# Optimization experiments

Hardware: AMD Instinct MI355X
Metric: run time of the kernel (lower is better)

## Reference

```python
import jax, jax.numpy as jnp
import numpy as np

B, T, P, D = 8, 2048, 4, 768

def setup_inputs() -> dict:
    key = jax.random.key(0)
    k1, k2, k3 = jax.random.split(key, 3)
    text_inputs = jax.random.normal(k1, (B, T, D), dtype=jnp.float32)
    sit_mask = jax.random.randint(k2, (B, T), 0, 2).astype(jnp.float32)
    proposition_matrix = jax.random.normal(k3, (B, T, P, D), dtype=jnp.float32)
    return {"text_inputs": text_inputs, "sit_mask": sit_mask, "proposition_matrix": proposition_matrix}

def reference(text_inputs, sit_mask, proposition_matrix):
    # D from proposition_matrix (matches text hidden dim), used for softmax scaling
    d = proposition_matrix.shape[-1]
    t = text_inputs.shape[1]
    # raw scores [B,T,T], scaled by 1/sqrt(D)
    scores = jnp.einsum('bid,bjd->bij', text_inputs, text_inputs) * (1.0 / jnp.sqrt(jnp.asarray(d, text_inputs.dtype)))
    # causal mask: strictly upper triangular -> -inf (tokens attend to self + past)
    causal = jnp.tril(jnp.ones((t, t), dtype=bool))  # [T,T]
    scores = jnp.where(causal[None, :, :], scores, -jnp.inf)
    weights = jax.nn.softmax(scores, axis=2)
    # padding mask via outer product of sit_mask; zero AFTER softmax (no renorm), as in original
    pad = (sit_mask[:, :, None] * sit_mask[:, None, :]) != 0  # [B,T,T]
    weights = jnp.where(pad, weights, jnp.zeros((), weights.dtype))
    out = jnp.einsum('bij,bjd->bid', weights, text_inputs)  # [B,T,D]
    # concat_self_hidden=True
    out = jnp.concatenate([out, text_inputs], axis=-1)  # [B,T,2D]
    return out
```

## Files before the change

kernel.cpp:

```cpp
#include <hip/hip_runtime.h>
#include <math.h>

constexpr int kT = 2048;
constexpr int kD = 768;
constexpr int kTileShorts = 16 * kD;
constexpr int kTilesPerBatch = kT / 16;

typedef __attribute__((ext_vector_type(8))) short short8;
typedef __attribute__((ext_vector_type(4))) float f32x4;
typedef __attribute__((ext_vector_type(16))) float f32x16;

#define FB(f) __builtin_bit_cast(unsigned, (f))
__device__ __forceinline__ unsigned pk_hi16(unsigned hi, unsigned lo) {
  return __builtin_amdgcn_perm(hi, lo, 0x07060302);
}
__device__ __forceinline__ unsigned pk_lo16(unsigned hi, unsigned lo) {
  return __builtin_amdgcn_perm(hi, lo, 0x05040100);
}

__device__ __forceinline__ void lds_barrier() {
  asm volatile("" ::: "memory");
  __builtin_amdgcn_s_waitcnt(0xC07F);
  __builtin_amdgcn_s_barrier();
  asm volatile("" ::: "memory");
}

__device__ __forceinline__ void gload_lds16(const void* g, void* l) {
  __builtin_amdgcn_global_load_lds(
      (const __attribute__((address_space(1))) unsigned int*)g,
      (__attribute__((address_space(3))) unsigned int*)l, 16, 0, 0);
}

__global__ __launch_bounds__(256) void prep_bf16(
    const float* __restrict__ x,
    unsigned short* __restrict__ xbf, unsigned short* __restrict__ xvt)
{
  const int tid = threadIdx.x;
  const int w = tid >> 6, l = tid & 63;
  const int l15 = l & 15, q4 = l >> 4;
  const int bt = (int)blockIdx.x;
  const float* xb = x + (size_t)bt * 16 * kD;
  unsigned short* ob = xbf + (size_t)bt * kTileShorts;
  unsigned short* ov = xvt + (size_t)bt * kTileShorts;

#pragma unroll
  for (int it = 0; it < 3; ++it) {
    const int dq = l15 + 16 * it + 48 * w;
    unsigned lo[4], hi[4];
#pragma unroll
    for (int jj = 0; jj < 4; ++jj) {
      const float4 f = *(const float4*)(xb + (size_t)(q4 + 4 * jj) * kD + 4 * dq);
      lo[jj] = pk_hi16(FB(f.y), FB(f.x));
      hi[jj] = pk_hi16(FB(f.w), FB(f.z));
    }
    const int dp = 4 * (l15 + 16 * it);
    const int g = dp >> 3, e0 = dp & 7;
#pragma unroll
    for (int jj = 0; jj < 4; ++jj) {
      const int j = q4 + 4 * jj;
      uint2 v; v.x = lo[jj]; v.y = hi[jj];
      *(uint2*)&ob[w * 3072 + j * 192 + ((g ^ (j & 7)) << 3) + e0] = v;
    }
    const int jb = (4 * q4) ^ (8 * ((dq >> 2) & 1));
    const int base = dq * 64 + jb;
    uint2 v;
    v.x = pk_lo16(lo[1], lo[0]); v.y = pk_lo16(lo[3], lo[2]);
    *(uint2*)&ov[base + ((0 ^ (dq & 3)) << 4)] = v;
    v.x = pk_hi16(lo[1], lo[0]); v.y = pk_hi16(lo[3], lo[2]);
    *(uint2*)&ov[base + ((1 ^ (dq & 3)) << 4)] = v;
    v.x = pk_lo16(hi[1], hi[0]); v.y = pk_lo16(hi[3], hi[2]);
    *(uint2*)&ov[base + ((2 ^ (dq & 3)) << 4)] = v;
    v.x = pk_hi16(hi[1], hi[0]); v.y = pk_hi16(hi[3], hi[2]);
    *(uint2*)&ov[base + ((3 ^ (dq & 3)) << 4)] = v;
  }
}

__global__ __launch_bounds__(256, 2) void attn_mfma5(
    const float* __restrict__ x, const float* __restrict__ mask,
    const unsigned short* __restrict__ xbf,
    const unsigned short* __restrict__ xvt,
    float* __restrict__ out, float* __restrict__ ml)
{
  const int tid = threadIdx.x;
  const int w = tid >> 6, l = tid & 63;
  const int l15 = l & 15, q4 = l >> 4;
  const int l31 = l & 31, h2 = l >> 5;

  const int bid = (int)blockIdx.x;
  const int b = bid & 7;
  const int s = bid >> 3;
  int qq, t0, t1, mode;
  if (s < 80) {
    int g = (s * 2) / 5;
    if (g > 31) g = 31;
    while (g < 31 && (2 * (g + 1) + ((g + 2) >> 1)) <= s) ++g;
    while (g > 0 && (2 * g + ((g + 1) >> 1)) > s) --g;
    const int r = s - (2 * g + ((g + 1) >> 1));
    if (r < 2) {
      qq = 63 - g;
      const int H = qq + 1;
      mode = 1 + r;
      t0 = (r == 0) ? 0 : H;
      t1 = (r == 0) ? H : 2 * H;
    } else {
      qq = 31 - (g >> 1);
      mode = 0; t0 = 0; t1 = 2 * qq + 2;
    }
  } else {
    qq = 15 - (s - 80);
    mode = 0; t0 = 0; t1 = 2 * qq + 2;
  }
  const int i0 = qq << 5;

  const float* xb = x + (size_t)b * kT * kD;
  const float* mrow = mask + (size_t)b * kT;
  const unsigned short* xbfB = xbf + (size_t)b * kTilesPerBatch * kTileShorts;
  const unsigned short* xvtB = xvt + (size_t)b * kTilesPerBatch * kTileShorts;

  __shared__ unsigned short xKc[12288];
  __shared__ unsigned short VTb[12288];
  __shared__ float sPart[2][4][16][36];
  __shared__ unsigned short Pm[2][32][16];
  __shared__ float corrS[2][32];
  __shared__ float invlS[32];
  __shared__ float msk[kT];

  {
    const char* msrc = (const char*)mrow + 2048 * w;
    char* mdst = (char*)&msk[512 * w];
    gload_lds16(msrc + 16 * l, mdst);
    gload_lds16(msrc + 1024 + 16 * l, mdst + 1024);
  }

  short8 qf[2][6];
#pragma unroll
  for (int mt = 0; mt < 2; ++mt) {
    const int tq = (i0 >> 4) + mt;
    const unsigned short* tp = xbfB + (size_t)tq * kTileShorts + w * 3072 + l15 * 192;
#pragma unroll
    for (int s6 = 0; s6 < 6; ++s6)
      qf[mt][s6] = *(const short8*)&tp[((4 * s6 + q4) ^ (l15 & 7)) << 3];
  }

  f32x16 o[6];
#pragma unroll
  for (int nt = 0; nt < 6; ++nt)
#pragma unroll
    for (int e = 0; e < 16; ++e) o[nt][e] = 0.0f;

  float mrun = -INFINITY, lrun = 0.0f;
  const float scale = 0.036084391824351615f;

  const int q = tid & 7, sr = tid >> 3;
  const int jA = (q >> 1) + 8 * (q & 1);
  const int irow = i0 + sr;

  const int D0 = 48 * w + (l31 >> 2);
  const int vtb_off0 = D0 * 64 + (((l31 & 3) ^ (D0 & 3)) << 4)
                     + ((8 * h2) ^ (8 * ((l31 >> 4) & 1)));

  auto stageK = [&](int t) {
    const unsigned short* src = xbfB + (size_t)t * kTileShorts + w * 3072 + 8 * l;
    unsigned short* dst = &xKc[w * 3072];
#pragma unroll
    for (int i = 0; i < 6; ++i) gload_lds16(src + 512 * i, dst + 512 * i);
  };
  auto stageV = [&](int t) {
    const unsigned short* src = xvtB + (size_t)t * kTileShorts + w * 3072 + 8 * l;
    unsigned short* dst = &VTb[w * 3072];
#pragma unroll
    for (int i = 0; i < 6; ++i) gload_lds16(src + 512 * i, dst + 512 * i);
  };

  stageK(t0);
  stageV(t0);
  asm volatile("s_waitcnt vmcnt(12)" ::: "memory");
  lds_barrier();

  for (int t = t0; t < t1; ++t) {
    const int par = t & 1;
    const int j0 = t << 4;

    asm volatile("s_waitcnt vmcnt(6)" ::: "memory");

    {
      f32x4 sf0, sf1;
#pragma unroll
      for (int e = 0; e < 4; ++e) { sf0[e] = 0.f; sf1[e] = 0.f; }
      const unsigned short* kbase = &xKc[w * 3072 + l15 * 192];
#pragma unroll
      for (int s6 = 0; s6 < 6; ++s6) {
        short8 kb = *(const short8*)&kbase[((4 * s6 + q4) ^ (l15 & 7)) << 3];
        sf0 = __builtin_amdgcn_mfma_f32_16x16x32_bf16(qf[0][s6], kb, sf0, 0, 0, 0);
        sf1 = __builtin_amdgcn_mfma_f32_16x16x32_bf16(qf[1][s6], kb, sf1, 0, 0, 0);
      }
      *(f32x4*)&sPart[par][w][l15][4 * q4]      = sf0;
      *(f32x4*)&sPart[par][w][l15][16 + 4 * q4] = sf1;
    }

    if (t + 1 < t1) {
      asm volatile("s_waitcnt lgkmcnt(0)" ::: "memory");
      stageK(t + 1);
    }
    lds_barrier();

    {
      float s0 = 0.f, s1 = 0.f;
#pragma unroll
      for (int ww = 0; ww < 4; ++ww) {
        s0 += sPart[par][ww][jA][sr];
        s1 += sPart[par][ww][jA + 4][sr];
      }
      const float mskA = msk[j0 + jA];
      const float mskB = msk[j0 + jA + 4];
      const int ja = j0 + jA, jb_ = j0 + jA + 4;
      float a0 = (ja  <= irow) ? s0 * scale : -INFINITY;
      float a1 = (jb_ <= irow) ? s1 * scale : -INFINITY;
      float loc = fmaxf(a0, a1);
      loc = fmaxf(loc, __shfl_xor(loc, 1, 64));
      loc = fmaxf(loc, __shfl_xor(loc, 2, 64));
      loc = fmaxf(loc, __shfl_xor(loc, 4, 64));
      const float mn = fmaxf(mrun, loc);
      const float corr = __expf(mrun - mn);
      const float p0 = __expf(a0 - mn);
      const float p1 = __expf(a1 - mn);
      float rs = p0 + p1;
      rs += __shfl_xor(rs, 1, 64);
      rs += __shfl_xor(rs, 2, 64);
      rs += __shfl_xor(rs, 4, 64);
      lrun = lrun * corr + rs;
      mrun = mn;
      const float w0 = (mskA != 0.f) ? p0 : 0.f;
      const float w1 = (mskB != 0.f) ? p1 : 0.f;
      *(unsigned*)&Pm[par][sr][2 * q] = pk_hi16(FB(w1), FB(w0));
      if (q == 0) corrS[par][sr] = corr;
    }
    lds_barrier();

    if (t + 1 < t1) { asm volatile("s_waitcnt vmcnt(6)" ::: "memory"); }
    else            { asm volatile("s_waitcnt vmcnt(0)" ::: "memory"); }

    {
      float cr[16];
#pragma unroll
      for (int e4 = 0; e4 < 4; ++e4) {
        f32x4 qd = *(const f32x4*)&corrS[par][8 * e4 + 4 * h2];
#pragma unroll
        for (int ee = 0; ee < 4; ++ee) cr[4 * e4 + ee] = qd[ee];
      }
#pragma unroll
      for (int nt = 0; nt < 6; ++nt)
#pragma unroll
        for (int e = 0; e < 16; ++e) o[nt][e] *= cr[e];
      short8 pa = *(const short8*)&Pm[par][l31][8 * h2];
#pragma unroll
      for (int nt = 0; nt < 6; ++nt) {
        short8 vb = *(const short8*)&VTb[vtb_off0 + 512 * nt];
        o[nt] = __builtin_amdgcn_mfma_f32_32x32x16_bf16(pa, vb, o[nt], 0, 0, 0);
      }
    }

    if (t + 1 < t1) {
      asm volatile("s_waitcnt lgkmcnt(0)" ::: "memory");
      stageV(t + 1);
    }
  }

  if (mode == 0) {
    if (q == 0) invlS[sr] = (msk[irow] != 0.f) ? 1.0f / lrun : 0.0f;
    lds_barrier();
    float il[16];
#pragma unroll
    for (int e4 = 0; e4 < 4; ++e4) {
      f32x4 qd = *(const f32x4*)&invlS[8 * e4 + 4 * h2];
#pragma unroll
      for (int ee = 0; ee < 4; ++ee) il[4 * e4 + ee] = qd[ee];
    }
    float* ob = out + (size_t)(b * kT + i0) * (2 * kD);
#pragma unroll
    for (int nt = 0; nt < 6; ++nt) {
      const int col = 192 * w + 32 * nt + l31;
#pragma unroll
      for (int e = 0; e < 16; ++e) {
        const int row = (e & 3) + 8 * (e >> 2) + 4 * h2;
        ob[(size_t)row * (2 * kD) + col] = o[nt][e] * il[e];
      }
    }
#pragma unroll
    for (int pass = 0; pass < 2; ++pass) {
      const int rr = (tid >> 4) + 16 * pass;
      const float* srcr = xb + (size_t)(i0 + rr) * kD;
      float* dstr = ob + (size_t)rr * (2 * kD) + kD;
#pragma unroll
      for (int it = 0; it < 12; ++it) {
        const int d4 = (tid & 15) + 16 * it;
        *(float4*)(dstr + 4 * d4) = *(const float4*)(srcr + 4 * d4);
      }
    }
  } else {
    float* ob = out + (size_t)(b * kT + i0) * (2 * kD) + ((mode == 2) ? kD : 0);
#pragma unroll
    for (int nt = 0; nt < 6; ++nt) {
      const int col = 192 * w + 32 * nt + l31;
#pragma unroll
      for (int e = 0; e < 16; ++e) {
        const int row = (e & 3) + 8 * (e >> 2) + 4 * h2;
        ob[(size_t)row * (2 * kD) + col] = o[nt][e];
      }
    }
    if (q == 0) {
      const int base = (((b * 32 + (qq - 32)) * 2 + (mode - 1)) * 64);
      ml[base + sr]      = mrun;
      ml[base + 32 + sr] = lrun;
    }
  }
}

__global__ __launch_bounds__(256) void combine_heavy(
    const float* __restrict__ x, const float* __restrict__ mask,
    const float* __restrict__ ml, float* __restrict__ out)
{
  const int tid = threadIdx.x;
  const int bid = (int)blockIdx.x;
  const int b = bid & 7;
  const int hq = bid >> 3;
  const int i0 = (hq + 32) << 5;
  const float* mrow = mask + (size_t)b * kT;
  const float* mlq = ml + (((size_t)b * 32 + hq) * 2) * 64;

  for (int r = 0; r < 32; ++r) {
    const int i = i0 + r;
    float* orow = out + (size_t)(b * kT + i) * (2 * kD);
    const float* xrow = x + (size_t)(b * kT + i) * kD;
    const float m1 = mlq[r],      l1 = mlq[32 + r];
    const float m2 = mlq[64 + r], l2 = mlq[96 + r];
    const float m = fmaxf(m1, m2);
    const float al = __expf(m1 - m), be = __expf(m2 - m);
    const float lsum = al * l1 + be * l2;
    const float gate = (mrow[i] != 0.f) ? 1.0f / lsum : 0.0f;
    const float ga = gate * al, gb = gate * be;
    if (tid < 192) {
      float4 o1 = *(const float4*)(orow + 4 * tid);
      float4 o2 = *(const float4*)(orow + kD + 4 * tid);
      float4 xv = *(const float4*)(xrow + 4 * tid);
      float4 fo;
      fo.x = ga * o1.x + gb * o2.x;
      fo.y = ga * o1.y + gb * o2.y;
      fo.z = ga * o1.z + gb * o2.z;
      fo.w = ga * o1.w + gb * o2.w;
      *(float4*)(orow + 4 * tid) = fo;
      *(float4*)(orow + kD + 4 * tid) = xv;
    }
  }
}

extern "C" void kernel_launch(void* const* d_in, const int* in_sizes, int n_in,
                              void* d_out, int out_size, void* d_ws, size_t ws_size,
                              hipStream_t stream) {
  const float* x    = (const float*)d_in[0];
  const float* mask = (const float*)d_in[1];
  float* out = (float*)d_out;
  unsigned short* xbf = (unsigned short*)d_ws;
  unsigned short* xvt = xbf + (size_t)8 * kTilesPerBatch * kTileShorts;
  float* ml = (float*)(xvt + (size_t)8 * kTilesPerBatch * kTileShorts);
  prep_bf16<<<dim3(8 * kTilesPerBatch), dim3(256), 0, stream>>>(x, xbf, xvt);
  attn_mfma5<<<dim3(768), dim3(256), 0, stream>>>(x, mask, xbf, xvt, out, ml);
  combine_heavy<<<dim3(256), dim3(256), 0, stream>>>(x, mask, ml, out);
}
```

Baseline: 446.3 us.

## Split attention block across 8 waves and load K/V tiles directly to registers

Doubles the block to 512 threads, with each wave owning half of a D-chunk for QK^T and 96 output columns for PV. The LDS staging of K and V tiles is replaced by direct global-to-register loads, prefetched one tile ahead, and s_setprio is wrapped around the MFMA sections. The goal is more waves per CU to hide latency, lower per-wave register pressure, and less LDS traffic. In exchange, the 8-way score partial reduction adds work, the double-buffered parity is gone, and each lane issues more global loads.

```diff
diff --git a/kernel.cpp b/kernel.cpp
--- a/kernel.cpp
+++ b/kernel.cpp
@@ -75,7 +75,7 @@
   }
 }
 
-__global__ __launch_bounds__(256, 2) void attn_mfma5(
+__global__ __launch_bounds__(512, 4) void attn_mfma6(
     const float* __restrict__ x, const float* __restrict__ mask,
     const unsigned short* __restrict__ xbf,
     const unsigned short* __restrict__ xvt,
@@ -85,6 +85,7 @@
   const int w = tid >> 6, l = tid & 63;
   const int l15 = l & 15, q4 = l >> 4;
   const int l31 = l & 31, h2 = l >> 5;
+  const int cch = w >> 1, hh = w & 1;
 
   const int bid = (int)blockIdx.x;
   const int b = bid & 7;
@@ -117,157 +118,137 @@
   const unsigned short* xbfB = xbf + (size_t)b * kTilesPerBatch * kTileShorts;
   const unsigned short* xvtB = xvt + (size_t)b * kTilesPerBatch * kTileShorts;
 
-  __shared__ unsigned short xKc[12288];
-  __shared__ unsigned short VTb[12288];
-  __shared__ float sPart[2][4][16][36];
-  __shared__ unsigned short Pm[2][32][16];
-  __shared__ float corrS[2][32];
-  __shared__ float invlS[32];
-  __shared__ float msk[kT];
-
+  __shared__ __attribute__((aligned(16))) float sPart[8][16][36];
+  __shared__ __attribute__((aligned(16))) unsigned short Pm[32][16];
+  __shared__ __attribute__((aligned(16))) float corrS[32];
+  __shared__ __attribute__((aligned(16))) float invlS[32];
+  __shared__ __attribute__((aligned(16))) float msk[kT];
+
+  gload_lds16((const char*)mrow + 1024 * w + 16 * l, (char*)&msk[256 * w]);
+
+  int koff[3];
+#pragma unroll
+  for (int s6 = 0; s6 < 3; ++s6) {
+    const int G = (4 * (3 * hh + s6) + q4) ^ (l15 & 7);
+    koff[s6] = cch * 3072 + l15 * 192 + G * 8;
+  }
+
+  short8 qf[2][3];
+#pragma unroll
+  for (int mt = 0; mt < 2; ++mt) {
+    const unsigned short* tp = xbfB + (size_t)((i0 >> 4) + mt) * kTileShorts;
+#pragma unroll
+    for (int s6 = 0; s6 < 3; ++s6)
+      qf[mt][s6] = *(const short8*)&tp[koff[s6]];
+  }
+
+  const int D0 = 24 * w + (l31 >> 2);
+  const int vtb_off0 = D0 * 64 + (((l31 & 3) ^ (D0 & 3)) << 4)
+                     + ((8 * h2) ^ (8 * ((l31 >> 4) & 1)));
+
+  short8 kb[3], vb[3];
   {
-    const char* msrc = (const char*)mrow + 2048 * w;
-    char* mdst = (char*)&msk[512 * w];
-    gload_lds16(msrc + 16 * l, mdst);
-    gload_lds16(msrc + 1024 + 16 * l, mdst + 1024);
-  }
-
-  short8 qf[2][6];
-#pragma unroll
-  for (int mt = 0; mt < 2; ++mt) {
-    const int tq = (i0 >> 4) + mt;
-    const unsigned short* tp = xbfB + (size_t)tq * kTileShorts + w * 3072 + l15 * 192;
-#pragma unroll
-    for (int s6 = 0; s6 < 6; ++s6)
-      qf[mt][s6] = *(const short8*)&tp[((4 * s6 + q4) ^ (l15 & 7)) << 3];
-  }
-
-  f32x16 o[6];
-#pragma unroll
-  for (int nt = 0; nt < 6; ++nt)
+    const unsigned short* kt = xbfB + (size_t)t0 * kTileShorts;
+    const unsigned short* vt = xvtB + (size_t)t0 * kTileShorts;
+#pragma unroll
+    for (int s6 = 0; s6 < 3; ++s6) kb[s6] = *(const short8*)&kt[koff[s6]];
+#pragma unroll
+    for (int nt = 0; nt < 3; ++nt) vb[nt] = *(const short8*)&vt[vtb_off0 + 512 * nt];
+  }
+
+  f32x16 o[3];
+#pragma unroll
+  for (int nt = 0; nt < 3; ++nt)
 #pragma unroll
     for (int e = 0; e < 16; ++e) o[nt][e] = 0.0f;
 
   float mrun = -INFINITY, lrun = 0.0f;
   const float scale = 0.036084391824351615f;
 
-  const int q = tid & 7, sr = tid >> 3;
-  const int jA = (q >> 1) + 8 * (q & 1);
-  const int irow = i0 + sr;
-
-  const int D0 = 48 * w + (l31 >> 2);
-  const int vtb_off0 = D0 * 64 + (((l31 & 3) ^ (D0 & 3)) << 4)
-                     + ((8 * h2) ^ (8 * ((l31 >> 4) & 1)));
-
-  auto stageK = [&](int t) {
-    const unsigned short* src = xbfB + (size_t)t * kTileShorts + w * 3072 + 8 * l;
-    unsigned short* dst = &xKc[w * 3072];
-#pragma unroll
-    for (int i = 0; i < 6; ++i) gload_lds16(src + 512 * i, dst + 512 * i);
-  };
-  auto stageV = [&](int t) {
-    const unsigned short* src = xvtB + (size_t)t * kTileShorts + w * 3072 + 8 * l;
-    unsigned short* dst = &VTb[w * 3072];
-#pragma unroll
-    for (int i = 0; i < 6; ++i) gload_lds16(src + 512 * i, dst + 512 * i);
-  };
-
-  stageK(t0);
-  stageV(t0);
-  asm volatile("s_waitcnt vmcnt(12)" ::: "memory");
-  lds_barrier();
+  const int r = tid >> 4, j = tid & 15;
+  const int irow = i0 + r;
+  const int cst = 4 * (j & 3) + 2 * (j >> 3) + ((j >> 2) & 1);
+
+  __syncthreads();
 
   for (int t = t0; t < t1; ++t) {
-    const int par = t & 1;
     const int j0 = t << 4;
-
-    asm volatile("s_waitcnt vmcnt(6)" ::: "memory");
 
     {
       f32x4 sf0, sf1;
 #pragma unroll
       for (int e = 0; e < 4; ++e) { sf0[e] = 0.f; sf1[e] = 0.f; }
-      const unsigned short* kbase = &xKc[w * 3072 + l15 * 192];
-#pragma unroll
-      for (int s6 = 0; s6 < 6; ++s6) {
-        short8 kb = *(const short8*)&kbase[((4 * s6 + q4) ^ (l15 & 7)) << 3];
-        sf0 = __builtin_amdgcn_mfma_f32_16x16x32_bf16(qf[0][s6], kb, sf0, 0, 0, 0);
-        sf1 = __builtin_amdgcn_mfma_f32_16x16x32_bf16(qf[1][s6], kb, sf1, 0, 0, 0);
-      }
-      *(f32x4*)&sPart[par][w][l15][4 * q4]      = sf0;
-      *(f32x4*)&sPart[par][w][l15][16 + 4 * q4] = sf1;
-    }
-
+      __builtin_amdgcn_s_setprio(1);
+#pragma unroll
+      for (int s6 = 0; s6 < 3; ++s6) {
+        sf0 = __builtin_amdgcn_mfma_f32_16x16x32_bf16(qf[0][s6], kb[s6], sf0, 0, 0, 0);
+        sf1 = __builtin_amdgcn_mfma_f32_16x16x32_bf16(qf[1][s6], kb[s6], sf1, 0, 0, 0);
+      }
+      __builtin_amdgcn_s_setprio(0);
+      *(f32x4*)&sPart[w][l15][4 * q4]      = sf0;
+      *(f32x4*)&sPart[w][l15][16 + 4 * q4] = sf1;
+    }
     if (t + 1 < t1) {
-      asm volatile("s_waitcnt lgkmcnt(0)" ::: "memory");
-      stageK(t + 1);
+      const unsigned short* kn = xbfB + (size_t)(t + 1) * kTileShorts;
+#pragma unroll
+      for (int s6 = 0; s6 < 3; ++s6) kb[s6] = *(const short8*)&kn[koff[s6]];
     }
     lds_barrier();
 
     {
-      float s0 = 0.f, s1 = 0.f;
-#pragma unroll
-      for (int ww = 0; ww < 4; ++ww) {
-        s0 += sPart[par][ww][jA][sr];
-        s1 += sPart[par][ww][jA + 4][sr];
-      }
-      const float mskA = msk[j0 + jA];
-      const float mskB = msk[j0 + jA + 4];
-      const int ja = j0 + jA, jb_ = j0 + jA + 4;
-      float a0 = (ja  <= irow) ? s0 * scale : -INFINITY;
-      float a1 = (jb_ <= irow) ? s1 * scale : -INFINITY;
-      float loc = fmaxf(a0, a1);
+      float ssum = 0.f;
+#pragma unroll
+      for (int ww = 0; ww < 8; ++ww) ssum += sPart[ww][j][r];
+      float a = (j0 + j <= irow) ? ssum * scale : -INFINITY;
+      float loc = a;
       loc = fmaxf(loc, __shfl_xor(loc, 1, 64));
       loc = fmaxf(loc, __shfl_xor(loc, 2, 64));
       loc = fmaxf(loc, __shfl_xor(loc, 4, 64));
+      loc = fmaxf(loc, __shfl_xor(loc, 8, 64));
       const float mn = fmaxf(mrun, loc);
       const float corr = __expf(mrun - mn);
-      const float p0 = __expf(a0 - mn);
-      const float p1 = __expf(a1 - mn);
-      float rs = p0 + p1;
+      const float p = __expf(a - mn);
+      float rs = p;
       rs += __shfl_xor(rs, 1, 64);
       rs += __shfl_xor(rs, 2, 64);
       rs += __shfl_xor(rs, 4, 64);
+      rs += __shfl_xor(rs, 8, 64);
       lrun = lrun * corr + rs;
       mrun = mn;
-      const float w0 = (mskA != 0.f) ? p0 : 0.f;
-      const float w1 = (mskB != 0.f) ? p1 : 0.f;
-      *(unsigned*)&Pm[par][sr][2 * q] = pk_hi16(FB(w1), FB(w0));
-      if (q == 0) corrS[par][sr] = corr;
+      const float wv = (msk[j0 + j] != 0.f) ? p : 0.f;
+      Pm[r][cst] = (unsigned short)(FB(wv) >> 16);
+      if (j == 0) corrS[r] = corr;
     }
     lds_barrier();
-
-    if (t + 1 < t1) { asm volatile("s_waitcnt vmcnt(6)" ::: "memory"); }
-    else            { asm volatile("s_waitcnt vmcnt(0)" ::: "memory"); }
 
     {
       float cr[16];
 #pragma unroll
       for (int e4 = 0; e4 < 4; ++e4) {
-        f32x4 qd = *(const f32x4*)&corrS[par][8 * e4 + 4 * h2];
+        f32x4 qd = *(const f32x4*)&corrS[8 * e4 + 4 * h2];
 #pragma unroll
         for (int ee = 0; ee < 4; ++ee) cr[4 * e4 + ee] = qd[ee];
       }
 #pragma unroll
-      for (int nt = 0; nt < 6; ++nt)
+      for (int nt = 0; nt < 3; ++nt)
 #pragma unroll
         for (int e = 0; e < 16; ++e) o[nt][e] *= cr[e];
-      short8 pa = *(const short8*)&Pm[par][l31][8 * h2];
-#pragma unroll
-      for (int nt = 0; nt < 6; ++nt) {
-        short8 vb = *(const short8*)&VTb[vtb_off0 + 512 * nt];
-        o[nt] = __builtin_amdgcn_mfma_f32_32x32x16_bf16(pa, vb, o[nt], 0, 0, 0);
-      }
-    }
-
+      short8 pa = *(const short8*)&Pm[l31][8 * h2];
+      __builtin_amdgcn_s_setprio(1);
+#pragma unroll
+      for (int nt = 0; nt < 3; ++nt)
+        o[nt] = __builtin_amdgcn_mfma_f32_32x32x16_bf16(pa, vb[nt], o[nt], 0, 0, 0);
+      __builtin_amdgcn_s_setprio(0);
+    }
     if (t + 1 < t1) {
-      asm volatile("s_waitcnt lgkmcnt(0)" ::: "memory");
-      stageV(t + 1);
+      const unsigned short* vn = xvtB + (size_t)(t + 1) * kTileShorts;
+#pragma unroll
+      for (int nt = 0; nt < 3; ++nt) vb[nt] = *(const short8*)&vn[vtb_off0 + 512 * nt];
     }
   }
 
   if (mode == 0) {
-    if (q == 0) invlS[sr] = (msk[irow] != 0.f) ? 1.0f / lrun : 0.0f;
+    if (j == 0) invlS[r] = (msk[irow] != 0.f) ? 1.0f / lrun : 0.0f;
     lds_barrier();
     float il[16];
 #pragma unroll
@@ -278,17 +259,16 @@
     }
     float* ob = out + (size_t)(b * kT + i0) * (2 * kD);
 #pragma unroll
-    for (int nt = 0; nt < 6; ++nt) {
-      const int col = 192 * w + 32 * nt + l31;
+    for (int nt = 0; nt < 3; ++nt) {
+      const int col = 96 * w + 32 * nt + l31;
 #pragma unroll
       for (int e = 0; e < 16; ++e) {
         const int row = (e & 3) + 8 * (e >> 2) + 4 * h2;
         ob[(size_t)row * (2 * kD) + col] = o[nt][e] * il[e];
       }
     }
-#pragma unroll
-    for (int pass = 0; pass < 2; ++pass) {
-      const int rr = (tid >> 4) + 16 * pass;
+    {
+      const int rr = tid >> 4;
       const float* srcr = xb + (size_t)(i0 + rr) * kD;
       float* dstr = ob + (size_t)rr * (2 * kD) + kD;
 #pragma unroll
@@ -300,18 +280,18 @@
   } else {
     float* ob = out + (size_t)(b * kT + i0) * (2 * kD) + ((mode == 2) ? kD : 0);
 #pragma unroll
-    for (int nt = 0; nt < 6; ++nt) {
-      const int col = 192 * w + 32 * nt + l31;
+    for (int nt = 0; nt < 3; ++nt) {
+      const int col = 96 * w + 32 * nt + l31;
 #pragma unroll
       for (int e = 0; e < 16; ++e) {
         const int row = (e & 3) + 8 * (e >> 2) + 4 * h2;
         ob[(size_t)row * (2 * kD) + col] = o[nt][e];
       }
     }
-    if (q == 0) {
+    if (j == 0) {
       const int base = (((b * 32 + (qq - 32)) * 2 + (mode - 1)) * 64);
-      ml[base + sr]      = mrun;
-      ml[base + 32 + sr] = lrun;
+      ml[base + r]      = mrun;
+      ml[base + 32 + r] = lrun;
     }
   }
 }
@@ -364,6 +344,6 @@
   unsigned short* xvt = xbf + (size_t)8 * kTilesPerBatch * kTileShorts;
   float* ml = (float*)(xvt + (size_t)8 * kTilesPerBatch * kTileShorts);
   prep_bf16<<<dim3(8 * kTilesPerBatch), dim3(256), 0, stream>>>(x, xbf, xvt);
-  attn_mfma5<<<dim3(768), dim3(256), 0, stream>>>(x, mask, xbf, xvt, out, ml);
+  attn_mfma6<<<dim3(768), dim3(512), 0, stream>>>(x, mask, xbf, xvt, out, ml);
   combine_heavy<<<dim3(256), dim3(256), 0, stream>>>(x, mask, ml, out);
 }
```

Result: slower. 540.6 us (+21.1%).

## Compute per-row online softmax redundantly per wave, removing one block barrier per tile

Applied to the files above, without the earlier changes.

The online-softmax step is restructured so each wave handles a whole query row per lane from transposed partial scores. This removes the Pm and corrS LDS exchange and the second block barrier in every key tile. Rescaling of the accumulators is skipped when no row max grows, and s_setprio is raised around the MFMA bursts. The V-transpose prep now goes through LDS and uses an unswizzled layout. The trade-off is extra redundant exp and max work per lane and possible bank conflicts on the plain VT layout.

```diff
diff --git a/kernel.cpp b/kernel.cpp
--- a/kernel.cpp
+++ b/kernel.cpp
@@ -13,9 +13,6 @@
 #define FB(f) __builtin_bit_cast(unsigned, (f))
 __device__ __forceinline__ unsigned pk_hi16(unsigned hi, unsigned lo) {
   return __builtin_amdgcn_perm(hi, lo, 0x07060302);
-}
-__device__ __forceinline__ unsigned pk_lo16(unsigned hi, unsigned lo) {
-  return __builtin_amdgcn_perm(hi, lo, 0x05040100);
 }
 
 __device__ __forceinline__ void lds_barrier() {
@@ -31,7 +28,7 @@
       (__attribute__((address_space(3))) unsigned int*)l, 16, 0, 0);
 }
 
-__global__ __launch_bounds__(256) void prep_bf16(
+__global__ __launch_bounds__(256) void prep_bf16b(
     const float* __restrict__ x,
     unsigned short* __restrict__ xbf, unsigned short* __restrict__ xvt)
 {
@@ -43,13 +40,17 @@
   unsigned short* ob = xbf + (size_t)bt * kTileShorts;
   unsigned short* ov = xvt + (size_t)bt * kTileShorts;
 
+  __shared__ float xs[16][772];
+
 #pragma unroll
   for (int it = 0; it < 3; ++it) {
     const int dq = l15 + 16 * it + 48 * w;
     unsigned lo[4], hi[4];
 #pragma unroll
     for (int jj = 0; jj < 4; ++jj) {
-      const float4 f = *(const float4*)(xb + (size_t)(q4 + 4 * jj) * kD + 4 * dq);
+      const int j = q4 + 4 * jj;
+      const float4 f = *(const float4*)(xb + (size_t)j * kD + 4 * dq);
+      *(float4*)&xs[j][4 * dq] = f;
       lo[jj] = pk_hi16(FB(f.y), FB(f.x));
       hi[jj] = pk_hi16(FB(f.w), FB(f.z));
     }
@@ -61,21 +62,23 @@
       uint2 v; v.x = lo[jj]; v.y = hi[jj];
       *(uint2*)&ob[w * 3072 + j * 192 + ((g ^ (j & 7)) << 3) + e0] = v;
     }
-    const int jb = (4 * q4) ^ (8 * ((dq >> 2) & 1));
-    const int base = dq * 64 + jb;
-    uint2 v;
-    v.x = pk_lo16(lo[1], lo[0]); v.y = pk_lo16(lo[3], lo[2]);
-    *(uint2*)&ov[base + ((0 ^ (dq & 3)) << 4)] = v;
-    v.x = pk_hi16(lo[1], lo[0]); v.y = pk_hi16(lo[3], lo[2]);
-    *(uint2*)&ov[base + ((1 ^ (dq & 3)) << 4)] = v;
-    v.x = pk_lo16(hi[1], hi[0]); v.y = pk_lo16(hi[3], hi[2]);
-    *(uint2*)&ov[base + ((2 ^ (dq & 3)) << 4)] = v;
-    v.x = pk_hi16(hi[1], hi[0]); v.y = pk_hi16(hi[3], hi[2]);
-    *(uint2*)&ov[base + ((3 ^ (dq & 3)) << 4)] = v;
-  }
-}
-
-__global__ __launch_bounds__(256, 2) void attn_mfma5(
+  }
+  __syncthreads();
+
+#pragma unroll
+  for (int cc = 0; cc < 6; ++cc) {
+    const int c = tid + 256 * cc;
+    const int d = c >> 1, kh = c & 1;
+    uint4 u;
+    u.x = pk_hi16(FB(xs[8 * kh + 1][d]), FB(xs[8 * kh + 0][d]));
+    u.y = pk_hi16(FB(xs[8 * kh + 3][d]), FB(xs[8 * kh + 2][d]));
+    u.z = pk_hi16(FB(xs[8 * kh + 5][d]), FB(xs[8 * kh + 4][d]));
+    u.w = pk_hi16(FB(xs[8 * kh + 7][d]), FB(xs[8 * kh + 6][d]));
+    *(uint4*)&ov[d * 16 + 8 * kh] = u;
+  }
+}
+
+__global__ __launch_bounds__(256, 2) void attn_mfma7(
     const float* __restrict__ x, const float* __restrict__ mask,
     const unsigned short* __restrict__ xbf,
     const unsigned short* __restrict__ xvt,
@@ -119,11 +122,9 @@
 
   __shared__ unsigned short xKc[12288];
   __shared__ unsigned short VTb[12288];
-  __shared__ float sPart[2][4][16][36];
-  __shared__ unsigned short Pm[2][32][16];
-  __shared__ float corrS[2][32];
-  __shared__ float invlS[32];
-  __shared__ float msk[kT];
+  __shared__ __attribute__((aligned(16))) float sPT[2][4][32][20];
+  __shared__ __attribute__((aligned(16))) float corrW[4][32];
+  __shared__ __attribute__((aligned(16))) float msk[kT];
 
   {
     const char* msrc = (const char*)mrow + 2048 * w;
@@ -150,14 +151,9 @@
 
   float mrun = -INFINITY, lrun = 0.0f;
   const float scale = 0.036084391824351615f;
-
-  const int q = tid & 7, sr = tid >> 3;
-  const int jA = (q >> 1) + 8 * (q & 1);
-  const int irow = i0 + sr;
-
-  const int D0 = 48 * w + (l31 >> 2);
-  const int vtb_off0 = D0 * 64 + (((l31 & 3) ^ (D0 & 3)) << 4)
-                     + ((8 * h2) ^ (8 * ((l31 >> 4) & 1)));
+  const int irow = i0 + l31;
+
+  const int vb_base = 3072 * w + 16 * l31 + 8 * h2;
 
   auto stageK = [&](int t) {
     const unsigned short* src = xbfB + (size_t)t * kTileShorts + w * 3072 + 8 * l;
@@ -174,28 +170,33 @@
 
   stageK(t0);
   stageV(t0);
-  asm volatile("s_waitcnt vmcnt(12)" ::: "memory");
+  asm volatile("s_waitcnt vmcnt(0)" ::: "memory");
   lds_barrier();
 
   for (int t = t0; t < t1; ++t) {
     const int par = t & 1;
     const int j0 = t << 4;
 
-    asm volatile("s_waitcnt vmcnt(6)" ::: "memory");
+    if (t > t0) { asm volatile("s_waitcnt vmcnt(6)" ::: "memory"); }
 
     {
       f32x4 sf0, sf1;
 #pragma unroll
       for (int e = 0; e < 4; ++e) { sf0[e] = 0.f; sf1[e] = 0.f; }
       const unsigned short* kbase = &xKc[w * 3072 + l15 * 192];
+      __builtin_amdgcn_s_setprio(1);
 #pragma unroll
       for (int s6 = 0; s6 < 6; ++s6) {
         short8 kb = *(const short8*)&kbase[((4 * s6 + q4) ^ (l15 & 7)) << 3];
         sf0 = __builtin_amdgcn_mfma_f32_16x16x32_bf16(qf[0][s6], kb, sf0, 0, 0, 0);
         sf1 = __builtin_amdgcn_mfma_f32_16x16x32_bf16(qf[1][s6], kb, sf1, 0, 0, 0);
       }
-      *(f32x4*)&sPart[par][w][l15][4 * q4]      = sf0;
-      *(f32x4*)&sPart[par][w][l15][16 + 4 * q4] = sf1;
+      __builtin_amdgcn_s_setprio(0);
+#pragma unroll
+      for (int e = 0; e < 4; ++e) {
+        sPT[par][w][4 * q4 + e][l15]      = sf0[e];
+        sPT[par][w][16 + 4 * q4 + e][l15] = sf1[e];
+      }
     }
 
     if (t + 1 < t1) {
@@ -204,60 +205,95 @@
     }
     lds_barrier();
 
+    short8 pa;
     {
-      float s0 = 0.f, s1 = 0.f;
-#pragma unroll
-      for (int ww = 0; ww < 4; ++ww) {
-        s0 += sPart[par][ww][jA][sr];
-        s1 += sPart[par][ww][jA + 4][sr];
-      }
-      const float mskA = msk[j0 + jA];
-      const float mskB = msk[j0 + jA + 4];
-      const int ja = j0 + jA, jb_ = j0 + jA + 4;
-      float a0 = (ja  <= irow) ? s0 * scale : -INFINITY;
-      float a1 = (jb_ <= irow) ? s1 * scale : -INFINITY;
-      float loc = fmaxf(a0, a1);
-      loc = fmaxf(loc, __shfl_xor(loc, 1, 64));
-      loc = fmaxf(loc, __shfl_xor(loc, 2, 64));
-      loc = fmaxf(loc, __shfl_xor(loc, 4, 64));
-      const float mn = fmaxf(mrun, loc);
-      const float corr = __expf(mrun - mn);
-      const float p0 = __expf(a0 - mn);
-      const float p1 = __expf(a1 - mn);
-      float rs = p0 + p1;
-      rs += __shfl_xor(rs, 1, 64);
-      rs += __shfl_xor(rs, 2, 64);
-      rs += __shfl_xor(rs, 4, 64);
-      lrun = lrun * corr + rs;
-      mrun = mn;
-      const float w0 = (mskA != 0.f) ? p0 : 0.f;
-      const float w1 = (mskB != 0.f) ? p1 : 0.f;
-      *(unsigned*)&Pm[par][sr][2 * q] = pk_hi16(FB(w1), FB(w0));
-      if (q == 0) corrS[par][sr] = corr;
-    }
-    lds_barrier();
+      f32x4 mk[4];
+#pragma unroll
+      for (int jg = 0; jg < 4; ++jg) mk[jg] = *(const f32x4*)&msk[j0 + 4 * jg];
+
+      float aj[16];
+#pragma unroll
+      for (int jg = 0; jg < 4; ++jg) {
+        f32x4 p0 = *(const f32x4*)&sPT[par][0][l31][4 * jg];
+        f32x4 p1 = *(const f32x4*)&sPT[par][1][l31][4 * jg];
+        f32x4 p2 = *(const f32x4*)&sPT[par][2][l31][4 * jg];
+        f32x4 p3 = *(const f32x4*)&sPT[par][3][l31][4 * jg];
+        f32x4 sm = (p0 + p1) + (p2 + p3);
+#pragma unroll
+        for (int m = 0; m < 4; ++m) {
+          const int j = 4 * jg + m;
+          aj[j] = (j0 + j <= irow) ? sm[m] * scale : -INFINITY;
+        }
+      }
+      float b8[8], c4[4];
+#pragma unroll
+      for (int k = 0; k < 8; ++k) b8[k] = fmaxf(aj[2 * k], aj[2 * k + 1]);
+#pragma unroll
+      for (int k = 0; k < 4; ++k) c4[k] = fmaxf(b8[2 * k], b8[2 * k + 1]);
+      const float rowmax = fmaxf(fmaxf(c4[0], c4[1]), fmaxf(c4[2], c4[3]));
+
+      if (!__all(rowmax <= mrun)) {
+        const float mn = fmaxf(mrun, rowmax);
+        const float corr = __expf(mrun - mn);
+        lrun *= corr;
+        mrun = mn;
+        corrW[w][l31] = corr;
+        asm volatile("s_waitcnt lgkmcnt(0)" ::: "memory");
+        float cr[16];
+#pragma unroll
+        for (int e4 = 0; e4 < 4; ++e4) {
+          f32x4 qd = *(const f32x4*)&corrW[w][8 * e4 + 4 * h2];
+#pragma unroll
+          for (int ee = 0; ee < 4; ++ee) cr[4 * e4 + ee] = qd[ee];
+        }
+#pragma unroll
+        for (int nt = 0; nt < 6; ++nt)
+#pragma unroll
+          for (int e = 0; e < 16; ++e) o[nt][e] *= cr[e];
+      }
+
+      float wv[16];
+      float r0 = 0.f, r1 = 0.f, r2 = 0.f, r3 = 0.f;
+#pragma unroll
+      for (int jg = 0; jg < 4; ++jg)
+#pragma unroll
+        for (int m = 0; m < 4; ++m) {
+          const int j = 4 * jg + m;
+          const float p = __expf(aj[j] - mrun);
+          if (m == 0) r0 += p; else if (m == 1) r1 += p;
+          else if (m == 2) r2 += p; else r3 += p;
+          wv[j] = (mk[jg][m] != 0.f) ? p : 0.f;
+        }
+      lrun += (r0 + r1) + (r2 + r3);
+
+      uint4 ulo, uhi;
+      ulo.x = pk_hi16(FB(wv[1]),  FB(wv[0]));
+      ulo.y = pk_hi16(FB(wv[3]),  FB(wv[2]));
+      ulo.z = pk_hi16(FB(wv[5]),  FB(wv[4]));
+      ulo.w = pk_hi16(FB(wv[7]),  FB(wv[6]));
+      uhi.x = pk_hi16(FB(wv[9]),  FB(wv[8]));
+      uhi.y = pk_hi16(FB(wv[11]), FB(wv[10]));
+      uhi.z = pk_hi16(FB(wv[13]), FB(wv[12]));
+      uhi.w = pk_hi16(FB(wv[15]), FB(wv[14]));
+      uint4 up;
+      up.x = h2 ? uhi.x : ulo.x;
+      up.y = h2 ? uhi.y : ulo.y;
+      up.z = h2 ? uhi.z : ulo.z;
+      up.w = h2 ? uhi.w : ulo.w;
+      pa = __builtin_bit_cast(short8, up);
+    }
 
     if (t + 1 < t1) { asm volatile("s_waitcnt vmcnt(6)" ::: "memory"); }
     else            { asm volatile("s_waitcnt vmcnt(0)" ::: "memory"); }
 
     {
-      float cr[16];
-#pragma unroll
-      for (int e4 = 0; e4 < 4; ++e4) {
-        f32x4 qd = *(const f32x4*)&corrS[par][8 * e4 + 4 * h2];
-#pragma unroll
-        for (int ee = 0; ee < 4; ++ee) cr[4 * e4 + ee] = qd[ee];
-      }
-#pragma unroll
-      for (int nt = 0; nt < 6; ++nt)
-#pragma unroll
-        for (int e = 0; e < 16; ++e) o[nt][e] *= cr[e];
-      short8 pa = *(const short8*)&Pm[par][l31][8 * h2];
+      __builtin_amdgcn_s_setprio(1);
 #pragma unroll
       for (int nt = 0; nt < 6; ++nt) {
-        short8 vb = *(const short8*)&VTb[vtb_off0 + 512 * nt];
+        short8 vb = *(const short8*)&VTb[vb_base + 512 * nt];
         o[nt] = __builtin_amdgcn_mfma_f32_32x32x16_bf16(pa, vb, o[nt], 0, 0, 0);
       }
+      __builtin_amdgcn_s_setprio(0);
     }
 
     if (t + 1 < t1) {
@@ -267,12 +303,12 @@
   }
 
   if (mode == 0) {
-    if (q == 0) invlS[sr] = (msk[irow] != 0.f) ? 1.0f / lrun : 0.0f;
-    lds_barrier();
+    corrW[w][l31] = (msk[irow] != 0.f) ? 1.0f / lrun : 0.0f;
+    asm volatile("s_waitcnt lgkmcnt(0)" ::: "memory");
     float il[16];
 #pragma unroll
     for (int e4 = 0; e4 < 4; ++e4) {
-      f32x4 qd = *(const f32x4*)&invlS[8 * e4 + 4 * h2];
+      f32x4 qd = *(const f32x4*)&corrW[w][8 * e4 + 4 * h2];
 #pragma unroll
       for (int ee = 0; ee < 4; ++ee) il[4 * e4 + ee] = qd[ee];
     }
@@ -308,10 +344,10 @@
         ob[(size_t)row * (2 * kD) + col] = o[nt][e];
       }
     }
-    if (q == 0) {
+    if (w == 0 && h2 == 0) {
       const int base = (((b * 32 + (qq - 32)) * 2 + (mode - 1)) * 64);
-      ml[base + sr]      = mrun;
-      ml[base + 32 + sr] = lrun;
+      ml[base + l31]      = mrun;
+      ml[base + 32 + l31] = lrun;
     }
   }
 }
@@ -363,7 +399,7 @@
   unsigned short* xbf = (unsigned short*)d_ws;
   unsigned short* xvt = xbf + (size_t)8 * kTilesPerBatch * kTileShorts;
   float* ml = (float*)(xvt + (size_t)8 * kTilesPerBatch * kTileShorts);
-  prep_bf16<<<dim3(8 * kTilesPerBatch), dim3(256), 0, stream>>>(x, xbf, xvt);
-  attn_mfma5<<<dim3(768), dim3(256), 0, stream>>>(x, mask, xbf, xvt, out, ml);
+  prep_bf16b<<<dim3(8 * kTilesPerBatch), dim3(256), 0, stream>>>(x, xbf, xvt);
+  attn_mfma7<<<dim3(768), dim3(256), 0, stream>>>(x, mask, xbf, xvt, out, ml);
   combine_heavy<<<dim3(256), dim3(256), 0, stream>>>(x, mask, ml, out);
 }
```

Result: slower. 477.4 us (+7.0%).

## Load V tiles directly into registers and shrink LDS to raise occupancy

Applied to the files above, without the earlier changes.

V fragments now go straight from global memory into registers and are prefetched one tile ahead, so the VTb LDS buffer and its staging waits disappear. The double-buffered sPart/Pm/corrS arrays become single-buffered and the float mask becomes a byte mask. Together these cut LDS use so launch bounds can target 3 blocks per CU. The block-to-work mapping is simplified to a plain split, the heavy rows split in two plus the light rows, and s_setprio is raised around the MFMA loops. The risks are higher register pressure from the 6 prefetched V fragments under the tighter launch bound, uncoalesced direct V loads, and possibly worse load balance from the new schedule order.

```diff
diff --git a/kernel.cpp b/kernel.cpp
--- a/kernel.cpp
+++ b/kernel.cpp
@@ -75,7 +75,7 @@
   }
 }
 
-__global__ __launch_bounds__(256, 2) void attn_mfma5(
+__global__ __launch_bounds__(256, 3) void attn_mfma8(
     const float* __restrict__ x, const float* __restrict__ mask,
     const unsigned short* __restrict__ xbf,
     const unsigned short* __restrict__ xvt,
@@ -90,24 +90,15 @@
   const int b = bid & 7;
   const int s = bid >> 3;
   int qq, t0, t1, mode;
-  if (s < 80) {
-    int g = (s * 2) / 5;
-    if (g > 31) g = 31;
-    while (g < 31 && (2 * (g + 1) + ((g + 2) >> 1)) <= s) ++g;
-    while (g > 0 && (2 * g + ((g + 1) >> 1)) > s) --g;
-    const int r = s - (2 * g + ((g + 1) >> 1));
-    if (r < 2) {
-      qq = 63 - g;
-      const int H = qq + 1;
-      mode = 1 + r;
-      t0 = (r == 0) ? 0 : H;
-      t1 = (r == 0) ? H : 2 * H;
-    } else {
-      qq = 31 - (g >> 1);
-      mode = 0; t0 = 0; t1 = 2 * qq + 2;
-    }
+  if (s < 64) {
+    const int c = (s < 32) ? s : (s - 32);
+    qq = 63 - c;
+    const int H = qq + 1;
+    mode = (s < 32) ? 1 : 2;
+    t0 = (s < 32) ? 0 : H;
+    t1 = (s < 32) ? H : 2 * H;
   } else {
-    qq = 15 - (s - 80);
+    qq = s - 64;
     mode = 0; t0 = 0; t1 = 2 * qq + 2;
   }
   const int i0 = qq << 5;
@@ -118,18 +109,19 @@
   const unsigned short* xvtB = xvt + (size_t)b * kTilesPerBatch * kTileShorts;
 
   __shared__ unsigned short xKc[12288];
-  __shared__ unsigned short VTb[12288];
-  __shared__ float sPart[2][4][16][36];
-  __shared__ unsigned short Pm[2][32][16];
-  __shared__ float corrS[2][32];
-  __shared__ float invlS[32];
-  __shared__ float msk[kT];
-
-  {
-    const char* msrc = (const char*)mrow + 2048 * w;
-    char* mdst = (char*)&msk[512 * w];
-    gload_lds16(msrc + 16 * l, mdst);
-    gload_lds16(msrc + 1024 + 16 * l, mdst + 1024);
+  __shared__ __attribute__((aligned(16))) float sPart[4][16][36];
+  __shared__ __attribute__((aligned(16))) unsigned short Pm[32][16];
+  __shared__ __attribute__((aligned(16))) float corrS[32];
+  __shared__ __attribute__((aligned(16))) float invlS[32];
+  __shared__ __attribute__((aligned(16))) unsigned char mskb[kT];
+
+#pragma unroll
+  for (int it = 0; it < 2; ++it) {
+    const int t4 = tid + 256 * it;
+    const float4 f = *(const float4*)(mrow + 4 * t4);
+    unsigned pk = (f.x != 0.f ? 1u : 0u) | (f.y != 0.f ? 0x100u : 0u)
+                | (f.z != 0.f ? 0x10000u : 0u) | (f.w != 0.f ? 0x1000000u : 0u);
+    *(unsigned*)&mskb[4 * t4] = pk;
   }
 
   short8 qf[2][6];
@@ -165,37 +157,34 @@
 #pragma unroll
     for (int i = 0; i < 6; ++i) gload_lds16(src + 512 * i, dst + 512 * i);
   };
-  auto stageV = [&](int t) {
-    const unsigned short* src = xvtB + (size_t)t * kTileShorts + w * 3072 + 8 * l;
-    unsigned short* dst = &VTb[w * 3072];
-#pragma unroll
-    for (int i = 0; i < 6; ++i) gload_lds16(src + 512 * i, dst + 512 * i);
-  };
 
   stageK(t0);
-  stageV(t0);
-  asm volatile("s_waitcnt vmcnt(12)" ::: "memory");
-  lds_barrier();
+  short8 vb[6];
+#pragma unroll
+  for (int nt = 0; nt < 6; ++nt)
+    vb[nt] = *(const short8*)&xvtB[(size_t)t0 * kTileShorts + vtb_off0 + 512 * nt];
+  __syncthreads();
 
   for (int t = t0; t < t1; ++t) {
-    const int par = t & 1;
     const int j0 = t << 4;
 
-    asm volatile("s_waitcnt vmcnt(6)" ::: "memory");
+    if (t > t0) { asm volatile("s_waitcnt vmcnt(6)" ::: "memory"); }
 
     {
       f32x4 sf0, sf1;
 #pragma unroll
       for (int e = 0; e < 4; ++e) { sf0[e] = 0.f; sf1[e] = 0.f; }
       const unsigned short* kbase = &xKc[w * 3072 + l15 * 192];
+      __builtin_amdgcn_s_setprio(1);
 #pragma unroll
       for (int s6 = 0; s6 < 6; ++s6) {
         short8 kb = *(const short8*)&kbase[((4 * s6 + q4) ^ (l15 & 7)) << 3];
         sf0 = __builtin_amdgcn_mfma_f32_16x16x32_bf16(qf[0][s6], kb, sf0, 0, 0, 0);
         sf1 = __builtin_amdgcn_mfma_f32_16x16x32_bf16(qf[1][s6], kb, sf1, 0, 0, 0);
       }
-      *(f32x4*)&sPart[par][w][l15][4 * q4]      = sf0;
-      *(f32x4*)&sPart[par][w][l15][16 + 4 * q4] = sf1;
+      __builtin_amdgcn_s_setprio(0);
+      *(f32x4*)&sPart[w][l15][4 * q4]      = sf0;
+      *(f32x4*)&sPart[w][l15][16 + 4 * q4] = sf1;
     }
 
     if (t + 1 < t1) {
@@ -208,11 +197,11 @@
       float s0 = 0.f, s1 = 0.f;
 #pragma unroll
       for (int ww = 0; ww < 4; ++ww) {
-        s0 += sPart[par][ww][jA][sr];
-        s1 += sPart[par][ww][jA + 4][sr];
-      }
-      const float mskA = msk[j0 + jA];
-      const float mskB = msk[j0 + jA + 4];
+        s0 += sPart[ww][jA][sr];
+        s1 += sPart[ww][jA + 4][sr];
+      }
+      const bool mA = mskb[j0 + jA] != 0;
+      const bool mB = mskb[j0 + jA + 4] != 0;
       const int ja = j0 + jA, jb_ = j0 + jA + 4;
       float a0 = (ja  <= irow) ? s0 * scale : -INFINITY;
       float a1 = (jb_ <= irow) ? s1 * scale : -INFINITY;
@@ -230,21 +219,18 @@
       rs += __shfl_xor(rs, 4, 64);
       lrun = lrun * corr + rs;
       mrun = mn;
-      const float w0 = (mskA != 0.f) ? p0 : 0.f;
-      const float w1 = (mskB != 0.f) ? p1 : 0.f;
-      *(unsigned*)&Pm[par][sr][2 * q] = pk_hi16(FB(w1), FB(w0));
-      if (q == 0) corrS[par][sr] = corr;
+      const float w0 = mA ? p0 : 0.f;
+      const float w1 = mB ? p1 : 0.f;
+      *(unsigned*)&Pm[sr][2 * q] = pk_hi16(FB(w1), FB(w0));
+      if (q == 0) corrS[sr] = corr;
     }
     lds_barrier();
-
-    if (t + 1 < t1) { asm volatile("s_waitcnt vmcnt(6)" ::: "memory"); }
-    else            { asm volatile("s_waitcnt vmcnt(0)" ::: "memory"); }
 
     {
       float cr[16];
 #pragma unroll
       for (int e4 = 0; e4 < 4; ++e4) {
-        f32x4 qd = *(const f32x4*)&corrS[par][8 * e4 + 4 * h2];
+        f32x4 qd = *(const f32x4*)&corrS[8 * e4 + 4 * h2];
 #pragma unroll
         for (int ee = 0; ee < 4; ++ee) cr[4 * e4 + ee] = qd[ee];
       }
@@ -252,22 +238,24 @@
       for (int nt = 0; nt < 6; ++nt)
 #pragma unroll
         for (int e = 0; e < 16; ++e) o[nt][e] *= cr[e];
-      short8 pa = *(const short8*)&Pm[par][l31][8 * h2];
-#pragma unroll
-      for (int nt = 0; nt < 6; ++nt) {
-        short8 vb = *(const short8*)&VTb[vtb_off0 + 512 * nt];
-        o[nt] = __builtin_amdgcn_mfma_f32_32x32x16_bf16(pa, vb, o[nt], 0, 0, 0);
-      }
+      short8 pa = *(const short8*)&Pm[l31][8 * h2];
+      __builtin_amdgcn_s_setprio(1);
+#pragma unroll
+      for (int nt = 0; nt < 6; ++nt)
+        o[nt] = __builtin_amdgcn_mfma_f32_32x32x16_bf16(pa, vb[nt], o[nt], 0, 0, 0);
+      __builtin_amdgcn_s_setprio(0);
     }
 
     if (t + 1 < t1) {
-      asm volatile("s_waitcnt lgkmcnt(0)" ::: "memory");
-      stageV(t + 1);
+      const unsigned short* vn = xvtB + (size_t)(t + 1) * kTileShorts + vtb_off0;
+#pragma unroll
+      for (int nt = 0; nt < 6; ++nt)
+        vb[nt] = *(const short8*)&vn[512 * nt];
     }
   }
 
   if (mode == 0) {
-    if (q == 0) invlS[sr] = (msk[irow] != 0.f) ? 1.0f / lrun : 0.0f;
+    if (q == 0) invlS[sr] = (mskb[irow] != 0) ? 1.0f / lrun : 0.0f;
     lds_barrier();
     float il[16];
 #pragma unroll
@@ -364,6 +352,6 @@
   unsigned short* xvt = xbf + (size_t)8 * kTilesPerBatch * kTileShorts;
   float* ml = (float*)(xvt + (size_t)8 * kTilesPerBatch * kTileShorts);
   prep_bf16<<<dim3(8 * kTilesPerBatch), dim3(256), 0, stream>>>(x, xbf, xvt);
-  attn_mfma5<<<dim3(768), dim3(256), 0, stream>>>(x, mask, xbf, xvt, out, ml);
+  attn_mfma8<<<dim3(768), dim3(256), 0, stream>>>(x, mask, xbf, xvt, out, ml);
   combine_heavy<<<dim3(256), dim3(256), 0, stream>>>(x, mask, ml, out);
 }
```

Result: slower. 662.9 us (+48.5%).
